# Kernel optimization log

Measured on AMD Instinct MI355X. Metric: run time of the kernel, lower is better.

Reference implementation:

```python
import jax, jax.numpy as jnp
import numpy as np

DIM = 256
N_HEADS = 4
B, N = 2, 4096


def setup_inputs() -> dict:
    key = jax.random.key(0)
    ks = jax.random.split(key, 10)
    s = DIM ** -0.5
    return {
        "x": jax.random.normal(ks[0], (B, N, DIM), dtype=jnp.float32),
        "q_w": jax.random.normal(ks[1], (DIM, DIM), dtype=jnp.float32) * s,
        "q_b": jnp.zeros((DIM,), dtype=jnp.float32),
        "k_w": jax.random.normal(ks[2], (DIM, DIM), dtype=jnp.float32) * s,
        "k_b": jnp.zeros((DIM,), dtype=jnp.float32),
        "v_w": jax.random.normal(ks[3], (DIM, DIM), dtype=jnp.float32) * s,
        "v_b": jnp.zeros((DIM,), dtype=jnp.float32),
        "o_w": jax.random.normal(ks[4], (DIM, DIM), dtype=jnp.float32) * s,
        "o_b": jnp.zeros((DIM,), dtype=jnp.float32),
        "tau": jnp.ones((1,), dtype=jnp.float32),
    }


def reference(x, q_w, q_b, k_w, k_b, v_w, v_b, o_w, o_b, tau):
    Bsz, Nlen, C = x.shape
    H = N_HEADS
    Dh = C // H
    scale = C ** -0.5  # source uses full dim, not head_dim
    Q = (x @ q_w.T + q_b).reshape(Bsz, Nlen, H, Dh)
    K = (x @ k_w.T + k_b).reshape(Bsz, Nlen, H, Dh)
    V = (x @ v_w.T + v_b).reshape(Bsz, Nlen, H, Dh)
    attn = jnp.einsum('bnhd,bmhd->bhnm', Q, K) * scale
    # soft-threshold gate: keep only |attn| > tau, then relu
    attn = jax.nn.relu(jnp.where(jnp.abs(attn) > tau, attn, 0.0))
    attn = jax.nn.softmax(attn, axis=-1)
    out = jnp.einsum('bhnm,bmhd->bnhd', attn, V).reshape(Bsz, Nlen, C)
    return out @ o_w.T + o_b
```

## Files before the change

### kernel.cpp

```cpp
#include <hip/hip_runtime.h>

#define SEQ   4096
#define CDIM  256
#define NHEAD 4
#define DHEAD 64
#define PSTRIDE 72
#define LOG2E 1.4426950408889634f

typedef float    f32x4 __attribute__((ext_vector_type(4)));
typedef _Float16 f16x8 __attribute__((ext_vector_type(8)));
typedef _Float16 f16x4 __attribute__((ext_vector_type(4)));
typedef _Float16 f16x2 __attribute__((ext_vector_type(2)));

__device__ __forceinline__ f16x8 cvt_frag(const float* __restrict__ p) {
    float4 f0 = *(const float4*)p;
    float4 f1 = *(const float4*)(p + 4);
    f16x8 r;
    r[0]=(_Float16)f0.x; r[1]=(_Float16)f0.y; r[2]=(_Float16)f0.z; r[3]=(_Float16)f0.w;
    r[4]=(_Float16)f1.x; r[5]=(_Float16)f1.y; r[6]=(_Float16)f1.z; r[7]=(_Float16)f1.w;
    return r;
}

__device__ __forceinline__ f16x2 pkrtz(float a, float b) {
    return __builtin_bit_cast(f16x2, __builtin_amdgcn_cvt_pkrtz(a, b));
}

__global__ __launch_bounds__(256) void sta_prep(
    const float* __restrict__ qw, const float* __restrict__ kw,
    const float* __restrict__ vw, const float* __restrict__ ow,
    _Float16* __restrict__ w16)
{
    const int mat = blockIdx.y;
    const float* src = (mat == 0) ? qw : (mat == 1) ? kw : (mat == 2) ? vw : ow;
    const int i = (blockIdx.x * 256 + threadIdx.x) * 8;
    *(f16x8*)(w16 + mat * 65536 + i) = cvt_frag(src + i);
}

__global__ __launch_bounds__(256) void sta_qkv(
    const float* __restrict__ x, const _Float16* __restrict__ w16,
    const float* __restrict__ qb, const float* __restrict__ kb, const float* __restrict__ vb,
    _Float16* __restrict__ Qo, _Float16* __restrict__ Ko, _Float16* __restrict__ Vo)
{
    const int wave = threadIdx.x >> 6;
    const int lane = threadIdx.x & 63;
    const int l15  = lane & 15;
    const int quad = lane >> 4;
    const int mat  = blockIdx.y;
    const int half = blockIdx.z;
    const int row0 = blockIdx.x * 64 + wave * 16;

    const _Float16* w    = w16 + mat * 65536;
    const float*    bias = (mat == 0) ? qb : (mat == 1) ? kb : vb;

    f16x8 xf[8];
    const float* xrow = x + (row0 + l15) * CDIM + quad * 8;
    #pragma unroll
    for (int ks = 0; ks < 8; ks++) xf[ks] = cvt_frag(xrow + ks * 32);

    #pragma unroll 1
    for (int ct = 0; ct < 8; ct++) {
        const int ctg = half * 8 + ct;
        const _Float16* wr = w + (ctg * 16 + l15) * CDIM + quad * 8;
        f32x4 acc = {0.f, 0.f, 0.f, 0.f};
        if (mat < 2) {
            #pragma unroll
            for (int ks = 0; ks < 8; ks++)
                acc = __builtin_amdgcn_mfma_f32_16x16x32_f16(*(const f16x8*)(wr + ks * 32), xf[ks], acc, 0, 0, 0);
            const float4 bv = *(const float4*)(bias + ctg * 16 + quad * 4);
            const int c0 = ctg * 16 + quad * 4;
            const int h = c0 >> 6, d0 = c0 & 63;
            const int grow = row0 + l15, b = grow >> 12, n = grow & (SEQ - 1);
            const float sc = (mat == 0) ? (0.0625f * LOG2E) : 1.0f;
            f16x4 o;
            o[0] = (_Float16)((acc[0] + bv.x) * sc);
            o[1] = (_Float16)((acc[1] + bv.y) * sc);
            o[2] = (_Float16)((acc[2] + bv.z) * sc);
            o[3] = (_Float16)((acc[3] + bv.w) * sc);
            _Float16* dst = ((mat == 0) ? Qo : Ko) + (((b * NHEAD + h) * SEQ + n) * DHEAD + d0);
            *(f16x4*)dst = o;
        } else {
            #pragma unroll
            for (int ks = 0; ks < 8; ks++)
                acc = __builtin_amdgcn_mfma_f32_16x16x32_f16(xf[ks], *(const f16x8*)(wr + ks * 32), acc, 0, 0, 0);
            const int c = ctg * 16 + l15;
            const int h = c >> 6, d = c & 63;
            const float bv = bias[c];
            const int grow0 = row0 + quad * 4, b = grow0 >> 12, n0 = grow0 & (SEQ - 1);
            f16x4 o;
            #pragma unroll
            for (int r = 0; r < 4; r++) o[r] = (_Float16)(acc[r] + bv);
            *(f16x4*)(Vo + (((b * NHEAD + h) * DHEAD + d) * SEQ + n0)) = o;
        }
    }
}

__global__ __launch_bounds__(64) void sta_attn(
    const _Float16* __restrict__ Q, const _Float16* __restrict__ K, const _Float16* __restrict__ Vt,
    const float* __restrict__ taup,
    float* __restrict__ Opart, float* __restrict__ lpart)
{
    __shared__ __align__(16) _Float16 pbuf[64 * PSTRIDE];

    const int lane = threadIdx.x;
    const int l15  = lane & 15;
    const int quad = lane >> 4;
    const int qt = blockIdx.x;
    const int bh = blockIdx.y;
    const int sp = blockIdx.z;
    const float tau2 = __builtin_bit_cast(float, __builtin_amdgcn_readfirstlane(
        __builtin_bit_cast(int, fmaxf(taup[0], 0.0f) * LOG2E)));

    const _Float16* Qb = Q  + bh * SEQ * DHEAD;
    const _Float16* Kb = K  + bh * SEQ * DHEAD;
    const _Float16* Vb = Vt + bh * DHEAD * SEQ;

    const int q0 = qt * 64;

    _Float16* __restrict__ pwb = pbuf + l15 * PSTRIDE + quad * 4;
    const _Float16* __restrict__ prb = pbuf + l15 * PSTRIDE + quad * 8;
    const _Float16* __restrict__ Krow = Kb + l15 * DHEAD + quad * 8;

    f16x8 qf[4][2];
    #pragma unroll
    for (int qb = 0; qb < 4; qb++)
        #pragma unroll
        for (int ks = 0; ks < 2; ks++)
            qf[qb][ks] = *(const f16x8*)(Qb + (q0 + qb * 16 + l15) * DHEAD + ks * 32 + quad * 8);

    f32x4 O[4][4];
    #pragma unroll
    for (int qb = 0; qb < 4; qb++)
        #pragma unroll
        for (int db = 0; db < 4; db++) O[qb][db] = (f32x4){0.f, 0.f, 0.f, 0.f};
    float rs[4] = {0.f, 0.f, 0.f, 0.f};

    const int kt_beg = sp * 11 - ((sp > 4) ? (sp - 4) : 0);
    const int kt_end = kt_beg + ((sp < 4) ? 11 : 10);
    #pragma unroll 1
    for (int kt = kt_beg; kt < kt_end; kt++) {
        const int kv0 = kt * 64;
        const _Float16* Kt = Krow + kv0 * DHEAD;

        #pragma unroll
        for (int kb = 0; kb < 4; kb++) {
            f16x8 k0 = *(const f16x8*)(Kt + kb * 16 * DHEAD);
            f16x8 k1 = *(const f16x8*)(Kt + kb * 16 * DHEAD + 32);
            #pragma unroll
            for (int qb = 0; qb < 4; qb++) {
                f32x4 a = {0.f, 0.f, 0.f, 0.f};
                a = __builtin_amdgcn_mfma_f32_16x16x32_f16(k0, qf[qb][0], a, 0, 0, 0);
                a = __builtin_amdgcn_mfma_f32_16x16x32_f16(k1, qf[qb][1], a, 0, 0, 0);
                float p0 = (a[0] > tau2) ? __builtin_amdgcn_exp2f(a[0]) : 1.0f;
                float p1 = (a[1] > tau2) ? __builtin_amdgcn_exp2f(a[1]) : 1.0f;
                float p2 = (a[2] > tau2) ? __builtin_amdgcn_exp2f(a[2]) : 1.0f;
                float p3 = (a[3] > tau2) ? __builtin_amdgcn_exp2f(a[3]) : 1.0f;
                rs[qb] += (p0 + p1) + (p2 + p3);
                uint2 pku;
                pku.x = __builtin_bit_cast(unsigned int, pkrtz(p0, p1));
                pku.y = __builtin_bit_cast(unsigned int, pkrtz(p2, p3));
                *(uint2*)(pwb + qb * 16 * PSTRIDE + kb * 16) = pku;
            }
        }

        #pragma unroll
        for (int ks = 0; ks < 2; ks++) {
            f16x8 pa[4];
            #pragma unroll
            for (int qb = 0; qb < 4; qb++)
                pa[qb] = *(const f16x8*)(prb + qb * 16 * PSTRIDE + ks * 32);
            #pragma unroll
            for (int db = 0; db < 4; db++) {
                f16x8 vf = *(const f16x8*)(Vb + (db * 16 + l15) * SEQ + kv0 + ks * 32 + quad * 8);
                #pragma unroll
                for (int qb = 0; qb < 4; qb++)
                    O[qb][db] = __builtin_amdgcn_mfma_f32_16x16x32_f16(pa[qb], vf, O[qb][db], 0, 0, 0);
            }
        }
    }

    #pragma unroll
    for (int qb = 0; qb < 4; qb++) {
        float v = rs[qb];
        v += __shfl_xor(v, 16);
        v += __shfl_xor(v, 32);
        rs[qb] = v;
    }
    float* Ob = Opart + (size_t)((sp * 8 + bh) * SEQ + q0) * DHEAD;
    #pragma unroll
    for (int qb = 0; qb < 4; qb++)
        #pragma unroll
        for (int db = 0; db < 4; db++)
            #pragma unroll
            for (int r = 0; r < 4; r++)
                Ob[(qb * 16 + quad * 4 + r) * DHEAD + db * 16 + l15] = O[qb][db][r];
    if (quad == 0) {
        #pragma unroll
        for (int qb = 0; qb < 4; qb++)
            lpart[(sp * 8 + bh) * SEQ + q0 + qb * 16 + l15] = rs[qb];
    }
}

__global__ __launch_bounds__(128) void sta_oproj2(
    const float* __restrict__ Opart, const float* __restrict__ lpart,
    const _Float16* __restrict__ w16o, const float* __restrict__ ob,
    float* __restrict__ out)
{
    const int wave = threadIdx.x >> 6;
    const int lane = threadIdx.x & 63;
    const int l15  = lane & 15;
    const int quad = lane >> 4;
    const int row0 = blockIdx.x * 32 + wave * 16;
    const int half = blockIdx.y;

    const int nglob = row0 + l15;
    const int b = nglob >> 12, n = nglob & (SEQ - 1);

    f16x8 af[8];
    #pragma unroll
    for (int h = 0; h < 4; h++) {
        const int bhh = b * NHEAD + h;
        float lsum = 0.f;
        #pragma unroll
        for (int s = 0; s < 6; s++) lsum += lpart[(s * 8 + bhh) * SEQ + n];
        const float inv = 1.0f / lsum;
        #pragma unroll
        for (int dp = 0; dp < 2; dp++) {
            const int dh0 = dp * 32 + quad * 8;
            float a0x=0.f,a0y=0.f,a0z=0.f,a0w=0.f,a1x=0.f,a1y=0.f,a1z=0.f,a1w=0.f;
            #pragma unroll
            for (int s = 0; s < 6; s++) {
                const float* p = Opart + (size_t)((s * 8 + bhh) * SEQ + n) * DHEAD + dh0;
                const float4 t0 = *(const float4*)p;
                const float4 t1 = *(const float4*)(p + 4);
                a0x += t0.x; a0y += t0.y; a0z += t0.z; a0w += t0.w;
                a1x += t1.x; a1y += t1.y; a1z += t1.z; a1w += t1.w;
            }
            f16x8 v;
            v[0] = (_Float16)(a0x * inv); v[1] = (_Float16)(a0y * inv);
            v[2] = (_Float16)(a0z * inv); v[3] = (_Float16)(a0w * inv);
            v[4] = (_Float16)(a1x * inv); v[5] = (_Float16)(a1y * inv);
            v[6] = (_Float16)(a1z * inv); v[7] = (_Float16)(a1w * inv);
            af[h * 2 + dp] = v;
        }
    }

    #pragma unroll 1
    for (int ct = 0; ct < 8; ct++) {
        const int ctg = half * 8 + ct;
        const _Float16* wr = w16o + (ctg * 16 + l15) * CDIM + quad * 8;
        f32x4 acc = {0.f, 0.f, 0.f, 0.f};
        #pragma unroll
        for (int ks = 0; ks < 8; ks++)
            acc = __builtin_amdgcn_mfma_f32_16x16x32_f16(*(const f16x8*)(wr + ks * 32), af[ks], acc, 0, 0, 0);
        const int c0 = ctg * 16 + quad * 4;
        const float4 bv = *(const float4*)(ob + c0);
        float4 res;
        res.x = acc[0] + bv.x; res.y = acc[1] + bv.y;
        res.z = acc[2] + bv.z; res.w = acc[3] + bv.w;
        *(float4*)(out + (size_t)nglob * CDIM + c0) = res;
    }
}

extern "C" void kernel_launch(void* const* d_in, const int* in_sizes, int n_in,
                              void* d_out, int out_size, void* d_ws, size_t ws_size,
                              hipStream_t stream) {
    const float* x   = (const float*)d_in[0];
    const float* qw  = (const float*)d_in[1];
    const float* qb  = (const float*)d_in[2];
    const float* kw  = (const float*)d_in[3];
    const float* kb  = (const float*)d_in[4];
    const float* vw  = (const float*)d_in[5];
    const float* vb  = (const float*)d_in[6];
    const float* ow  = (const float*)d_in[7];
    const float* ob  = (const float*)d_in[8];
    const float* tau = (const float*)d_in[9];

    _Float16* w16 = (_Float16*)d_ws;
    _Float16* Q   = w16 + 262144;
    _Float16* K   = Q + 2097152;
    _Float16* Vt  = K + 2097152;
    float* Opart  = (float*)(Vt + 2097152);
    float* lpart  = Opart + 12582912;

    sta_prep  <<<dim3(32, 4),      256, 0, stream>>>(qw, kw, vw, ow, w16);
    sta_qkv   <<<dim3(128, 3, 2),  256, 0, stream>>>(x, w16, qb, kb, vb, Q, K, Vt);
    sta_attn  <<<dim3(64, 8, 6),    64, 0, stream>>>(Q, K, Vt, tau, Opart, lpart);
    sta_oproj2<<<dim3(256, 2),     128, 0, stream>>>(Opart, lpart, w16 + 3 * 65536, ob, (float*)d_out);
}
```

Baseline: 205.1 us.

## Use four KV splits and double-buffer the P tile in LDS

Reduces the attention split-KV factor from 6 to 4, so each block processes 16 KV tiles. The grid drops from 3072 to 2048 single-wave blocks and the oproj reduction reads less partial data. It also alternates between two LDS P buffers so consecutive tiles can overlap the write of one tile with reads of the other without a hazard. The trade-off is fewer blocks in flight, which lowers parallelism on a 256-CU device, and twice the LDS per block.

```diff
diff --git a/kernel.cpp b/kernel.cpp
--- a/kernel.cpp
+++ b/kernel.cpp
@@ -99,7 +99,7 @@
     const float* __restrict__ taup,
     float* __restrict__ Opart, float* __restrict__ lpart)
 {
-    __shared__ __align__(16) _Float16 pbuf[64 * PSTRIDE];
+    __shared__ __align__(16) _Float16 pbuf[2 * 64 * PSTRIDE];
 
     const int lane = threadIdx.x;
     const int l15  = lane & 15;
@@ -116,9 +116,11 @@
 
     const int q0 = qt * 64;
 
-    _Float16* __restrict__ pwb = pbuf + l15 * PSTRIDE + quad * 4;
-    const _Float16* __restrict__ prb = pbuf + l15 * PSTRIDE + quad * 8;
-    const _Float16* __restrict__ Krow = Kb + l15 * DHEAD + quad * 8;
+    _Float16* pw0 = pbuf + l15 * PSTRIDE + quad * 4;
+    const _Float16* pr0 = pbuf + l15 * PSTRIDE + quad * 8;
+    _Float16* pw1 = pw0 + 64 * PSTRIDE;
+    const _Float16* pr1 = pr0 + 64 * PSTRIDE;
+    const _Float16* Krow = Kb + l15 * DHEAD + quad * 8;
 
     f16x8 qf[4][2];
     #pragma unroll
@@ -134,13 +136,8 @@
         for (int db = 0; db < 4; db++) O[qb][db] = (f32x4){0.f, 0.f, 0.f, 0.f};
     float rs[4] = {0.f, 0.f, 0.f, 0.f};
 
-    const int kt_beg = sp * 11 - ((sp > 4) ? (sp - 4) : 0);
-    const int kt_end = kt_beg + ((sp < 4) ? 11 : 10);
-    #pragma unroll 1
-    for (int kt = kt_beg; kt < kt_end; kt++) {
-        const int kv0 = kt * 64;
+    auto tile = [&](int kv0, _Float16* pw, const _Float16* pr) {
         const _Float16* Kt = Krow + kv0 * DHEAD;
-
         #pragma unroll
         for (int kb = 0; kb < 4; kb++) {
             f16x8 k0 = *(const f16x8*)(Kt + kb * 16 * DHEAD);
@@ -155,19 +152,19 @@
                 float p2 = (a[2] > tau2) ? __builtin_amdgcn_exp2f(a[2]) : 1.0f;
                 float p3 = (a[3] > tau2) ? __builtin_amdgcn_exp2f(a[3]) : 1.0f;
                 rs[qb] += (p0 + p1) + (p2 + p3);
-                uint2 pku;
-                pku.x = __builtin_bit_cast(unsigned int, pkrtz(p0, p1));
-                pku.y = __builtin_bit_cast(unsigned int, pkrtz(p2, p3));
-                *(uint2*)(pwb + qb * 16 * PSTRIDE + kb * 16) = pku;
+                f16x2 lo = pkrtz(p0, p1);
+                f16x2 hi = pkrtz(p2, p3);
+                f16x4 pk;
+                pk[0] = lo[0]; pk[1] = lo[1]; pk[2] = hi[0]; pk[3] = hi[1];
+                *(f16x4*)(pw + qb * 16 * PSTRIDE + kb * 16) = pk;
             }
         }
-
         #pragma unroll
         for (int ks = 0; ks < 2; ks++) {
             f16x8 pa[4];
             #pragma unroll
             for (int qb = 0; qb < 4; qb++)
-                pa[qb] = *(const f16x8*)(prb + qb * 16 * PSTRIDE + ks * 32);
+                pa[qb] = *(const f16x8*)(pr + qb * 16 * PSTRIDE + ks * 32);
             #pragma unroll
             for (int db = 0; db < 4; db++) {
                 f16x8 vf = *(const f16x8*)(Vb + (db * 16 + l15) * SEQ + kv0 + ks * 32 + quad * 8);
@@ -176,6 +173,13 @@
                     O[qb][db] = __builtin_amdgcn_mfma_f32_16x16x32_f16(pa[qb], vf, O[qb][db], 0, 0, 0);
             }
         }
+    };
+
+    const int kvb = sp * 16 * 64;
+    #pragma unroll 1
+    for (int kp = 0; kp < 8; kp++) {
+        tile(kvb + (kp * 2 + 0) * 64, pw0, pr0);
+        tile(kvb + (kp * 2 + 1) * 64, pw1, pr1);
     }
 
     #pragma unroll
@@ -221,14 +225,14 @@
         const int bhh = b * NHEAD + h;
         float lsum = 0.f;
         #pragma unroll
-        for (int s = 0; s < 6; s++) lsum += lpart[(s * 8 + bhh) * SEQ + n];
+        for (int s = 0; s < 4; s++) lsum += lpart[(s * 8 + bhh) * SEQ + n];
         const float inv = 1.0f / lsum;
         #pragma unroll
         for (int dp = 0; dp < 2; dp++) {
             const int dh0 = dp * 32 + quad * 8;
             float a0x=0.f,a0y=0.f,a0z=0.f,a0w=0.f,a1x=0.f,a1y=0.f,a1z=0.f,a1w=0.f;
             #pragma unroll
-            for (int s = 0; s < 6; s++) {
+            for (int s = 0; s < 4; s++) {
                 const float* p = Opart + (size_t)((s * 8 + bhh) * SEQ + n) * DHEAD + dh0;
                 const float4 t0 = *(const float4*)p;
                 const float4 t1 = *(const float4*)(p + 4);
@@ -280,10 +284,10 @@
     _Float16* K   = Q + 2097152;
     _Float16* Vt  = K + 2097152;
     float* Opart  = (float*)(Vt + 2097152);
-    float* lpart  = Opart + 12582912;
+    float* lpart  = Opart + 8388608;
 
     sta_prep  <<<dim3(32, 4),      256, 0, stream>>>(qw, kw, vw, ow, w16);
     sta_qkv   <<<dim3(128, 3, 2),  256, 0, stream>>>(x, w16, qb, kb, vb, Q, K, Vt);
-    sta_attn  <<<dim3(64, 8, 6),    64, 0, stream>>>(Q, K, Vt, tau, Opart, lpart);
+    sta_attn  <<<dim3(64, 8, 4),    64, 0, stream>>>(Q, K, Vt, tau, Opart, lpart);
     sta_oproj2<<<dim3(256, 2),     128, 0, stream>>>(Opart, lpart, w16 + 3 * 65536, ob, (float*)d_out);
 }
```

New measurement: 218.3 us. 6.4% more time.
